# Kernel optimization log

Hardware: AMD Instinct MI355X
Metric: run time of the kernel (lower is better)

The kernel has to match this reference:

```python
import jax, jax.numpy as jnp
import numpy as np

EPS = 1e-5

def setup_inputs() -> dict:
    key = jax.random.key(0)
    ks = jax.random.split(key, 12)
    N, d0, d1, d2, qh, qo = 8192, 128, 256, 256, 128, 1
    state = jax.random.normal(ks[0], (N, d0), dtype=jnp.float32)
    adjacent_matrix = jax.random.uniform(ks[1], (N, N), dtype=jnp.float32)
    s = 0.05
    return {
        "state": state,
        "adjacent_matrix": adjacent_matrix,
        "gamma": jnp.ones((d0,), jnp.float32),
        "beta": jnp.zeros((d0,), jnp.float32),
        "W1": jax.random.normal(ks[2], (d0, d1), jnp.float32) * s,
        "b1": jnp.zeros((d1,), jnp.float32),
        "W2": jax.random.normal(ks[3], (d1, d2), jnp.float32) * s,
        "b2": jnp.zeros((d2,), jnp.float32),
        "Wq1": jax.random.normal(ks[4], (d2, qh), jnp.float32) * s,
        "bq1": jnp.zeros((qh,), jnp.float32),
        "Wq2": jax.random.normal(ks[5], (qh, qo), jnp.float32) * s,
        "bq2": jnp.zeros((qo,), jnp.float32),
    }


def reference(state, adjacent_matrix, gamma, beta, W1, b1, W2, b2, Wq1, bq1, Wq2, bq2):
    # LinkBatchNorm: BatchNorm1d over node (batch) axis, training-mode statistics
    mean = jnp.mean(state, axis=0)
    var = jnp.var(state, axis=0)
    x = (state - mean) * jax.lax.rsqrt(var + EPS) * gamma + beta  # [N, d0]
    # GraphCNN: two layers of relu(A @ X @ W + b)
    h = jax.nn.relu(adjacent_matrix @ (x @ W1) + b1)   # [N, d1]
    h = jax.nn.relu(adjacent_matrix @ (h @ W2) + b2)   # [N, d2]
    # QNetwork: per-node MLP -> Q value
    q = jax.nn.relu(h @ Wq1 + bq1) @ Wq2 + bq2         # [N, 1]
    return q
```

## Files before the change

kernel.cpp:

```cpp
#include <hip/hip_runtime.h>
#include <stdint.h>

#define NN 8192
#define D0 128
#define D1 256
#define D2 256
#define QH 128
#define EPSV 1e-5f

using bf16x8 = __attribute__((ext_vector_type(8))) __bf16;
using f32x4  = __attribute__((ext_vector_type(4))) float;

__device__ __forceinline__ unsigned short f2bf(float f) {
    union { float f; unsigned int u; } v; v.f = f;
    unsigned int r = v.u + 0x7FFFu + ((v.u >> 16) & 1u);
    return (unsigned short)(r >> 16);
}
__device__ __forceinline__ float bf2f(unsigned short h) {
    union { unsigned int u; float f; } v; v.u = ((unsigned int)h) << 16;
    return v.f;
}
__device__ __forceinline__ unsigned pkbf(float a, float b) {
    unsigned r;
    asm("v_cvt_pk_bf16_f32 %0, %1, %2" : "=v"(r) : "v"(a), "v"(b));
    return r;
}
__device__ __forceinline__ void async_ld16(const void* g, void* l) {
    __builtin_amdgcn_global_load_lds(
        (__attribute__((address_space(1))) void*)(g),
        (__attribute__((address_space(3))) void*)(l), 16, 0, 0);
}

__global__ void k_stats(const float* __restrict__ state,
                        float* __restrict__ psum, float* __restrict__ psq,
                        float* __restrict__ acc4k, float* __restrict__ rsA) {
    int j = threadIdx.x;
    int b = blockIdx.x;
    int gid = b * 128 + j;
    if (gid < 8192) rsA[gid] = 0.f;
    if (gid < 1024) acc4k[gid] = 0.f;
    const float* p = state + (size_t)b * 32 * D0 + j;
    float s = 0.f, sq = 0.f;
#pragma unroll 4
    for (int r = 0; r < 32; ++r) { float x = p[(size_t)r * D0]; s += x; sq += x * x; }
    psum[b * D0 + j] = s;
    psq [b * D0 + j] = sq;
}

__global__ void k_finalize(const float* __restrict__ psum, const float* __restrict__ psq,
                           const float* __restrict__ gamma, const float* __restrict__ beta,
                           const float* __restrict__ W1,
                           float* __restrict__ scale, float* __restrict__ shift,
                           float* __restrict__ c1) {
    __shared__ float s_shift[D0];
    int t = threadIdx.x;
    if (t < D0) {
        float s = 0.f, sq = 0.f;
        for (int b = 0; b < 256; ++b) { s += psum[b * D0 + t]; sq += psq[b * D0 + t]; }
        float mean = s * (1.0f / NN);
        float var  = sq * (1.0f / NN) - mean * mean;
        float sc = gamma[t] * rsqrtf(var + EPSV);
        float sh = beta[t] - mean * sc;
        scale[t] = sc; shift[t] = sh; s_shift[t] = sh;
    }
    __syncthreads();
    float acc = 0.f;
    for (int k = 0; k < D0; ++k) acc += s_shift[k] * W1[(size_t)k * D1 + t];
    c1[t] = acc;
}

__global__ void k_prep_weights(const float* __restrict__ W1, const float* __restrict__ W2,
                               const float* __restrict__ scale,
                               unsigned short* __restrict__ W1st,
                               unsigned short* __restrict__ W2t) {
    int idx = blockIdx.x * 256 + threadIdx.x;
    if (idx < 32768) {
        int n = idx >> 7, k = idx & 127;
        W1st[idx] = f2bf(W1[(size_t)k * D1 + n] * scale[k]);
    } else {
        int i = idx - 32768; int n = i >> 8, k = i & 255;
        W2t[i] = f2bf(W2[(size_t)k * D2 + n]);
    }
}

__global__ __launch_bounds__(256) void k_castA_T(const float* __restrict__ A,
                                                 unsigned short* __restrict__ AbfT,
                                                 float* __restrict__ rs) {
    int t = threadIdx.x;
    int row = blockIdx.x * 128 + (t >> 1);
    int off = (t & 1) * 16;
    const float* ap = A + (size_t)row * NN + blockIdx.y * 2048 + off;
    unsigned short* op = AbfT + (size_t)(blockIdx.y * 64) * ((size_t)NN * 32)
                              + (size_t)row * 32 + off;
    const size_t PL = (size_t)NN * 32;
    float s = 0.f;
    for (int kt = 0; kt < 64; ++kt) {
        const float* p = ap + kt * 32;
        float4 v0 = *(const float4*)(p);
        float4 v1 = *(const float4*)(p + 4);
        float4 v2 = *(const float4*)(p + 8);
        float4 v3 = *(const float4*)(p + 12);
        s += v0.x + v0.y + v0.z + v0.w + v1.x + v1.y + v1.z + v1.w
           + v2.x + v2.y + v2.z + v2.w + v3.x + v3.y + v3.z + v3.w;
        uint4 u0 = { pkbf(v0.x, v0.y), pkbf(v0.z, v0.w), pkbf(v1.x, v1.y), pkbf(v1.z, v1.w) };
        uint4 u1 = { pkbf(v2.x, v2.y), pkbf(v2.z, v2.w), pkbf(v3.x, v3.y), pkbf(v3.z, v3.w) };
        *(uint4*)(op + (size_t)kt * PL) = u0;
        *(uint4*)(op + (size_t)kt * PL + 8) = u1;
    }
    s += __shfl_xor(s, 1, 64);
    if ((t & 1) == 0) atomicAdd(rs + row, s);
}

template <int N, int K, bool A_FP32, bool BIAS>
__global__ __launch_bounds__(256, 4) void k_small_gemm(
        const void* __restrict__ Aptr, const unsigned short* __restrict__ Bt,
        const float* __restrict__ bias, unsigned short* __restrict__ out) {
    constexpr int WN = N / 4;
    constexpr int NJ = WN / 16;
    constexpr int BI = N / 64;
    __shared__ unsigned short Alds[32 * 32];
    __shared__ unsigned short Blds[N * 32];
    int t = threadIdx.x, lane = t & 63, w = t >> 6;
    int m0 = blockIdx.x * 32;
    int lr = lane & 15, lk = (lane >> 4) * 8;
    int wc = w * WN;
    f32x4 acc[2][NJ] = {};

    for (int kk = 0; kk < K; kk += 32) {
        __syncthreads();
        if constexpr (A_FP32) {
            const float* A = (const float*)Aptr;
            int row = t >> 3, kc = (t & 7) * 4;
            float4 v = *(const float4*)(A + (size_t)(m0 + row) * K + kk + kc);
            uint2 p;
            p.x = ((unsigned)f2bf(v.y) << 16) | f2bf(v.x);
            p.y = ((unsigned)f2bf(v.w) << 16) | f2bf(v.z);
            *(uint2*)&Alds[row * 32 + kc] = p;
        } else {
            if (w < 2) {
                const unsigned short* A = (const unsigned short*)Aptr;
                int row = w * 16 + (lane >> 2);
                async_ld16(A + (size_t)(m0 + row) * K + kk + (lane & 3) * 8, &Alds[w * 512]);
            }
        }
#pragma unroll
        for (int i = 0; i < BI; ++i) {
            int n = w * WN + i * 16 + (lane >> 2);
            async_ld16(Bt + (size_t)n * K + kk + (lane & 3) * 8, &Blds[(w * WN + i * 16) * 32]);
        }
        __syncthreads();
        bf16x8 a[2], b[NJ];
#pragma unroll
        for (int i = 0; i < 2; ++i) a[i] = *(const bf16x8*)&Alds[(i * 16 + lr) * 32 + lk];
#pragma unroll
        for (int j = 0; j < NJ; ++j) b[j] = *(const bf16x8*)&Blds[(wc + j * 16 + lr) * 32 + lk];
#pragma unroll
        for (int i = 0; i < 2; ++i)
#pragma unroll
            for (int j = 0; j < NJ; ++j)
                acc[i][j] = __builtin_amdgcn_mfma_f32_16x16x32_bf16(a[i], b[j], acc[i][j], 0, 0, 0);
    }
    int q = lane >> 4;
#pragma unroll
    for (int j = 0; j < NJ; ++j) {
        int n = wc + j * 16 + lr;
        float bv = 0.f;
        if constexpr (BIAS) bv = bias[n];
#pragma unroll
        for (int i = 0; i < 2; ++i) {
#pragma unroll
            for (int r = 0; r < 4; ++r) {
                int m = m0 + i * 16 + q * 4 + r;
                out[(size_t)m * N + n] = f2bf(acc[i][j][r] + bv);
            }
        }
    }
}

__global__ void k_transpose(const unsigned short* __restrict__ in, unsigned short* __restrict__ out,
                            float* __restrict__ colsum) {
    __shared__ unsigned short tile[64 * 68];
    __shared__ float cp[4][64];
    int t = threadIdx.x;
    int r0 = blockIdx.x * 64, c0 = blockIdx.y * 64;
#pragma unroll
    for (int p = 0; p < 4; ++p) {
        int row = (t >> 4) + p * 16, col = (t & 15) * 4;
        *(ushort4*)&tile[row * 68 + col] = *(const ushort4*)&in[(size_t)(r0 + row) * 256 + c0 + col];
    }
    __syncthreads();
    int n = t >> 2;
#pragma unroll
    for (int s = 0; s < 2; ++s) {
        int mo = (t & 3) * 16 + s * 8;
        unsigned short v[8];
#pragma unroll
        for (int e = 0; e < 8; ++e) v[e] = tile[(mo + e) * 68 + n];
        int kt = (r0 + mo) >> 5;
        *(uint4*)&out[(size_t)kt * 8192 + (c0 + n) * 32 + (mo & 31)] = *(const uint4*)v;
    }
    int col = t & 63, gg = t >> 6;
    float s = 0.f;
#pragma unroll
    for (int r = 0; r < 16; ++r) s += bf2f(tile[(gg * 16 + r) * 68 + col]);
    cp[gg][col] = s;
    __syncthreads();
    if (t < 64) atomicAdd(colsum + c0 + t, cp[0][t] + cp[1][t] + cp[2][t] + cp[3][t]);
}

__global__ __launch_bounds__(512, 4) void k_big_gemm7(
        const unsigned short* __restrict__ AbfT, const unsigned short* __restrict__ Ytb,
        float* __restrict__ Cp) {
    __shared__ unsigned short Alds[3][128 * 32];
    __shared__ unsigned short Blds[3][256 * 32];
    int t = threadIdx.x, lane = t & 63, w = t >> 6;
    int m0 = blockIdx.x * 128;
    int kt0 = blockIdx.y * 32;
    int wr = (w & 1) * 64, wc = (w >> 1) * 64;
    int lr = lane & 15, q = lane >> 4;
    f32x4 acc[4][4] = {};

    const size_t AS = (size_t)NN * 32;
    const int    BS = 256 * 32;
    int srow = lane >> 2;
    int hsw = (lane & 3) ^ ((srow ^ (srow >> 2)) & 3);
    const unsigned short* agp = AbfT + (size_t)kt0 * AS + (size_t)(m0 + w * 16 + srow) * 32 + hsw * 8;
    const unsigned short* bg0 = Ytb + (size_t)kt0 * BS + (w * 32 + srow) * 32 + hsw * 8;
    const unsigned short* bg1 = bg0 + 16 * 32;
    unsigned short* aL  = &Alds[0][0] + w * 512;
    unsigned short* bL0 = &Blds[0][0] + w * 1024;
    unsigned short* bL1 = bL0 + 512;
    int xsr = (lr ^ (lr >> 2)) & 3;
    int lks = ((q ^ xsr) & 3) * 8;

#pragma unroll
    for (int pt = 0; pt < 2; ++pt) {
        async_ld16(agp + (size_t)pt * AS, aL  + pt * 4096);
        async_ld16(bg0 + (size_t)pt * BS, bL0 + pt * 8192);
        async_ld16(bg1 + (size_t)pt * BS, bL1 + pt * 8192);
    }
    asm volatile("s_waitcnt vmcnt(3)" ::: "memory");
    __builtin_amdgcn_s_barrier();
    __builtin_amdgcn_sched_barrier(0);

    int cur = 0;
#define GEMM7_COMPUTE(BUF)                                                              \
    {                                                                                   \
        const unsigned short* Ab = &Alds[0][0] + (BUF) * 4096;                          \
        const unsigned short* Bb = &Blds[0][0] + (BUF) * 8192;                          \
        bf16x8 a[4];                                                                    \
        _Pragma("unroll")                                                               \
        for (int i = 0; i < 4; ++i) a[i] = *(const bf16x8*)&Ab[(wr + i * 16 + lr) * 32 + lks]; \
        _Pragma("unroll")                                                               \
        for (int j = 0; j < 4; ++j) {                                                   \
            bf16x8 b = *(const bf16x8*)&Bb[(wc + j * 16 + lr) * 32 + lks];              \
            _Pragma("unroll")                                                           \
            for (int i = 0; i < 4; ++i)                                                 \
                acc[i][j] = __builtin_amdgcn_mfma_f32_16x16x32_bf16(a[i], b, acc[i][j], 0, 0, 0); \
        }                                                                               \
    }

#pragma unroll 3
    for (int it = 0; it < 30; ++it) {
        int nb = cur + 2; if (nb >= 3) nb -= 3;
        async_ld16(agp + (size_t)(it + 2) * AS, aL  + nb * 4096);
        async_ld16(bg0 + (size_t)(it + 2) * BS, bL0 + nb * 8192);
        async_ld16(bg1 + (size_t)(it + 2) * BS, bL1 + nb * 8192);
        GEMM7_COMPUTE(cur)
        asm volatile("s_waitcnt vmcnt(3)" ::: "memory");
        __builtin_amdgcn_s_barrier();
        __builtin_amdgcn_sched_barrier(0);
        ++cur; if (cur >= 3) cur = 0;
    }
    GEMM7_COMPUTE(cur)
    asm volatile("s_waitcnt vmcnt(0)" ::: "memory");
    __builtin_amdgcn_s_barrier();
    __builtin_amdgcn_sched_barrier(0);
    ++cur; if (cur >= 3) cur = 0;
    GEMM7_COMPUTE(cur)
#undef GEMM7_COMPUTE

    float* outp = Cp + (size_t)blockIdx.y * NN * 256;
#pragma unroll
    for (int i = 0; i < 4; ++i)
#pragma unroll
        for (int j = 0; j < 4; ++j) {
            int n = wc + j * 16 + lr;
#pragma unroll
            for (int r = 0; r < 4; ++r) {
                int m = m0 + wr + i * 16 + q * 4 + r;
                outp[(size_t)m * 256 + n] = acc[i][j][r];
            }
        }
}

__global__ void k_s2(const float* __restrict__ colB, const float* __restrict__ colH1,
                     const float* __restrict__ W2, float* __restrict__ s2) {
    int n = threadIdx.x;
    float acc = 0.f;
    for (int k = 0; k < 256; ++k) acc += colH1[k] * W2[(size_t)k * 256 + n];
    s2[n] = colB[n] - acc;
}

__global__ __launch_bounds__(256) void k_reduce8(
        const float* __restrict__ Cp, const float* __restrict__ rsA,
        const float* __restrict__ bias, const float* __restrict__ sn,
        unsigned short* __restrict__ out, float* __restrict__ colH1) {
    __shared__ float rs_s[16];
    __shared__ float cs[4][256];
    int t = threadIdx.x;
    int m0 = blockIdx.x * 16;
    const size_t S = (size_t)NN * 256;
    if (t < 16) rs_s[t] = rsA[m0 + t] * (1.0f / 8192.0f);
    __syncthreads();
    int g = t >> 6, cq = (t & 63) * 4;
    float4 snv = *(const float4*)(sn + cq);
    float4 bv  = *(const float4*)(bias + cq);
    float c0 = 0.f, c1a = 0.f, c2 = 0.f, c3 = 0.f;
#pragma unroll
    for (int r4 = 0; r4 < 4; ++r4) {
        int row = g * 4 + r4;
        size_t base = (size_t)(m0 + row) * 256 + cq;
        float4 a = {0.f, 0.f, 0.f, 0.f};
#pragma unroll
        for (int s = 0; s < 8; ++s) {
            float4 p = *(const float4*)(Cp + (size_t)s * S + base);
            a.x += p.x; a.y += p.y; a.z += p.z; a.w += p.w;
        }
        float rsv = rs_s[row];
        float x0 = fmaxf(a.x + bv.x - rsv * snv.x, 0.f);
        float x1 = fmaxf(a.y + bv.y - rsv * snv.y, 0.f);
        float x2 = fmaxf(a.z + bv.z - rsv * snv.z, 0.f);
        float x3 = fmaxf(a.w + bv.w - rsv * snv.w, 0.f);
        ushort4 o; o.x = f2bf(x0); o.y = f2bf(x1); o.z = f2bf(x2); o.w = f2bf(x3);
        *(ushort4*)(out + base) = o;
        c0 += x0; c1a += x1; c2 += x2; c3 += x3;
    }
    cs[g][cq] = c0; cs[g][cq + 1] = c1a; cs[g][cq + 2] = c2; cs[g][cq + 3] = c3;
    __syncthreads();
    float tot = cs[0][t] + cs[1][t] + cs[2][t] + cs[3][t];
    atomicAdd(colH1 + t, tot);
}

__global__ __launch_bounds__(256) void k_reduce_qhead(
        const float* __restrict__ Cp, const float* __restrict__ rsA,
        const float* __restrict__ bias, const float* __restrict__ sn,
        const float* __restrict__ Wq1, const float* __restrict__ bq1,
        const float* __restrict__ Wq2, const float* __restrict__ bq2,
        float* __restrict__ out) {
    __shared__ float sh[16][256];
    __shared__ float rs_s[16];
    __shared__ float red[4][8];
    int t = threadIdx.x;
    int m0 = blockIdx.x * 16;
    const size_t S = (size_t)NN * 256;
    if (t < 16) rs_s[t] = rsA[m0 + t] * (1.0f / 8192.0f);
    __syncthreads();
    int g = t >> 6, cq = (t & 63) * 4;
    float4 snv = *(const float4*)(sn + cq);
    float4 bv  = *(const float4*)(bias + cq);
#pragma unroll
    for (int r4 = 0; r4 < 4; ++r4) {
        int row = g * 4 + r4;
        size_t base = (size_t)(m0 + row) * 256 + cq;
        float4 a = {0.f, 0.f, 0.f, 0.f};
#pragma unroll
        for (int s = 0; s < 8; ++s) {
            float4 p = *(const float4*)(Cp + (size_t)s * S + base);
            a.x += p.x; a.y += p.y; a.z += p.z; a.w += p.w;
        }
        float rsv = rs_s[row];
        float4 o;
        o.x = fmaxf(a.x + bv.x - rsv * snv.x, 0.f);
        o.y = fmaxf(a.y + bv.y - rsv * snv.y, 0.f);
        o.z = fmaxf(a.z + bv.z - rsv * snv.z, 0.f);
        o.w = fmaxf(a.w + bv.w - rsv * snv.w, 0.f);
        *(float4*)&sh[row][cq] = o;
    }
    __syncthreads();
    int h = t & 127, rg = t >> 7;
    float acc[8] = {};
    const float* wq = Wq1 + h;
    for (int n4 = 0; n4 < 64; ++n4) {
        int n = n4 * 4;
        float wa = wq[(size_t)(n + 0) * QH];
        float wb = wq[(size_t)(n + 1) * QH];
        float wcc = wq[(size_t)(n + 2) * QH];
        float wd = wq[(size_t)(n + 3) * QH];
#pragma unroll
        for (int r = 0; r < 8; ++r) {
            float4 sv = *(const float4*)&sh[rg * 8 + r][n];
            acc[r] = fmaf(sv.x, wa, fmaf(sv.y, wb, fmaf(sv.z, wcc, fmaf(sv.w, wd, acc[r]))));
        }
    }
    float b1v = bq1[h], w2v = Wq2[h];
    int wid = t >> 6, lane = t & 63;
#pragma unroll
    for (int r = 0; r < 8; ++r) {
        float v = fmaxf(acc[r] + b1v, 0.f) * w2v;
#pragma unroll
        for (int d = 32; d > 0; d >>= 1) v += __shfl_down(v, d, 64);
        if (lane == 0) red[wid][r] = v;
    }
    __syncthreads();
    if (t < 16) {
        int rg2 = t >> 3, r = t & 7;
        out[m0 + rg2 * 8 + r] = red[rg2 * 2][r] + red[rg2 * 2 + 1][r] + bq2[0];
    }
}

extern "C" void kernel_launch(void* const* d_in, const int* in_sizes, int n_in,
                              void* d_out, int out_size, void* d_ws, size_t ws_size,
                              hipStream_t stream) {
    const float* state = (const float*)d_in[0];
    const float* adj   = (const float*)d_in[1];
    const float* gamma = (const float*)d_in[2];
    const float* beta  = (const float*)d_in[3];
    const float* W1    = (const float*)d_in[4];
    const float* b1    = (const float*)d_in[5];
    const float* W2    = (const float*)d_in[6];
    const float* b2    = (const float*)d_in[7];
    const float* Wq1   = (const float*)d_in[8];
    const float* bq1   = (const float*)d_in[9];
    const float* Wq2   = (const float*)d_in[10];
    const float* bq2   = (const float*)d_in[11];
    float* out = (float*)d_out;

    char* ws = (char*)d_ws;
    float* psum  = (float*)(ws + 0);
    float* psq   = (float*)(ws + 131072);
    float* scale = (float*)(ws + 262144);
    float* shift = (float*)(ws + 262656);
    float* c1    = (float*)(ws + 263168);
    float* colA  = (float*)(ws + 264192);
    float* colB  = (float*)(ws + 265216);
    float* colH1 = (float*)(ws + 266240);
    float* s2    = (float*)(ws + 267264);
    unsigned short* W1st = (unsigned short*)(ws + 268288);
    unsigned short* W2t  = (unsigned short*)(ws + 333824);
    unsigned short* Ybuf = (unsigned short*)(ws + (size_t)1  * (1u << 20));
    unsigned short* Ytb  = (unsigned short*)(ws + (size_t)5  * (1u << 20));
    unsigned short* Hbuf = (unsigned short*)(ws + (size_t)9  * (1u << 20));
    float*          rsA  = (float*)(ws + (size_t)14 * (1u << 20));
    float*          Cp   = (float*)(ws + (size_t)22 * (1u << 20));
    unsigned short* AbfT = (unsigned short*)(ws + (size_t)128 * (1u << 20));

    k_stats<<<256, 128, 0, stream>>>(state, psum, psq, colA, rsA);
    k_finalize<<<1, 256, 0, stream>>>(psum, psq, gamma, beta, W1, scale, shift, c1);
    k_prep_weights<<<384, 256, 0, stream>>>(W1, W2, scale, W1st, W2t);
    k_castA_T<<<dim3(64, 4), 256, 0, stream>>>(adj, AbfT, rsA);

    k_small_gemm<256, 128, true, true><<<256, 256, 0, stream>>>(state, W1st, c1, Ybuf);
    k_transpose<<<dim3(128, 4), 256, 0, stream>>>(Ybuf, Ytb, colA);
    k_big_gemm7<<<dim3(64, 8), 512, 0, stream>>>(AbfT, Ytb, Cp);
    k_reduce8<<<512, 256, 0, stream>>>(Cp, rsA, b1, colA, Hbuf, colH1);

    k_small_gemm<256, 256, false, false><<<256, 256, 0, stream>>>(Hbuf, W2t, nullptr, Ybuf);
    k_transpose<<<dim3(128, 4), 256, 0, stream>>>(Ybuf, Ytb, colB);
    k_s2<<<1, 256, 0, stream>>>(colB, colH1, W2, s2);
    k_big_gemm7<<<dim3(64, 8), 512, 0, stream>>>(AbfT, Ytb, Cp);
    k_reduce_qhead<<<512, 256, 0, stream>>>(Cp, rsA, b2, s2, Wq1, bq1, Wq2, bq2, out);
}
```

Baseline: 613.7 us.

## Replace LDS-staged big GEMM with register-direct global loads and N-split grid

Rewrites the large adjacency GEMM to skip shared-memory staging: each wave loads its bf16 MFMA fragments directly from global memory into registers with a two-stage register double buffer. The block tile shrinks to 128x128 with 256 threads, and a new grid dimension splits the 256 output columns in two. This removes the LDS writes, reads and barriers. In exchange, global/L2 traffic rises because fragments are no longer shared across waves through LDS, and load latency is hidden only by the register prefetch and occupancy.

```diff
diff --git a/kernel.cpp b/kernel.cpp
--- a/kernel.cpp
+++ b/kernel.cpp
@@ -208,84 +208,59 @@
     if (t < 64) atomicAdd(colsum + c0 + t, cp[0][t] + cp[1][t] + cp[2][t] + cp[3][t]);
 }
 
-__global__ __launch_bounds__(512, 4) void k_big_gemm7(
+__global__ __launch_bounds__(256, 3) void k_big_gemm8(
         const unsigned short* __restrict__ AbfT, const unsigned short* __restrict__ Ytb,
         float* __restrict__ Cp) {
-    __shared__ unsigned short Alds[3][128 * 32];
-    __shared__ unsigned short Blds[3][256 * 32];
     int t = threadIdx.x, lane = t & 63, w = t >> 6;
     int m0 = blockIdx.x * 128;
-    int kt0 = blockIdx.y * 32;
+    int n0 = blockIdx.y * 128;
+    int kt0 = blockIdx.z * 32;
     int wr = (w & 1) * 64, wc = (w >> 1) * 64;
     int lr = lane & 15, q = lane >> 4;
     f32x4 acc[4][4] = {};
 
     const size_t AS = (size_t)NN * 32;
-    const int    BS = 256 * 32;
-    int srow = lane >> 2;
-    int hsw = (lane & 3) ^ ((srow ^ (srow >> 2)) & 3);
-    const unsigned short* agp = AbfT + (size_t)kt0 * AS + (size_t)(m0 + w * 16 + srow) * 32 + hsw * 8;
-    const unsigned short* bg0 = Ytb + (size_t)kt0 * BS + (w * 32 + srow) * 32 + hsw * 8;
-    const unsigned short* bg1 = bg0 + 16 * 32;
-    unsigned short* aL  = &Alds[0][0] + w * 512;
-    unsigned short* bL0 = &Blds[0][0] + w * 1024;
-    unsigned short* bL1 = bL0 + 512;
-    int xsr = (lr ^ (lr >> 2)) & 3;
-    int lks = ((q ^ xsr) & 3) * 8;
-
-#pragma unroll
-    for (int pt = 0; pt < 2; ++pt) {
-        async_ld16(agp + (size_t)pt * AS, aL  + pt * 4096);
-        async_ld16(bg0 + (size_t)pt * BS, bL0 + pt * 8192);
-        async_ld16(bg1 + (size_t)pt * BS, bL1 + pt * 8192);
-    }
-    asm volatile("s_waitcnt vmcnt(3)" ::: "memory");
-    __builtin_amdgcn_s_barrier();
-    __builtin_amdgcn_sched_barrier(0);
-
-    int cur = 0;
-#define GEMM7_COMPUTE(BUF)                                                              \
-    {                                                                                   \
-        const unsigned short* Ab = &Alds[0][0] + (BUF) * 4096;                          \
-        const unsigned short* Bb = &Blds[0][0] + (BUF) * 8192;                          \
-        bf16x8 a[4];                                                                    \
-        _Pragma("unroll")                                                               \
-        for (int i = 0; i < 4; ++i) a[i] = *(const bf16x8*)&Ab[(wr + i * 16 + lr) * 32 + lks]; \
-        _Pragma("unroll")                                                               \
-        for (int j = 0; j < 4; ++j) {                                                   \
-            bf16x8 b = *(const bf16x8*)&Bb[(wc + j * 16 + lr) * 32 + lks];              \
-            _Pragma("unroll")                                                           \
-            for (int i = 0; i < 4; ++i)                                                 \
-                acc[i][j] = __builtin_amdgcn_mfma_f32_16x16x32_bf16(a[i], b, acc[i][j], 0, 0, 0); \
-        }                                                                               \
-    }
-
-#pragma unroll 3
-    for (int it = 0; it < 30; ++it) {
-        int nb = cur + 2; if (nb >= 3) nb -= 3;
-        async_ld16(agp + (size_t)(it + 2) * AS, aL  + nb * 4096);
-        async_ld16(bg0 + (size_t)(it + 2) * BS, bL0 + nb * 8192);
-        async_ld16(bg1 + (size_t)(it + 2) * BS, bL1 + nb * 8192);
-        GEMM7_COMPUTE(cur)
-        asm volatile("s_waitcnt vmcnt(3)" ::: "memory");
-        __builtin_amdgcn_s_barrier();
-        __builtin_amdgcn_sched_barrier(0);
-        ++cur; if (cur >= 3) cur = 0;
-    }
-    GEMM7_COMPUTE(cur)
-    asm volatile("s_waitcnt vmcnt(0)" ::: "memory");
-    __builtin_amdgcn_s_barrier();
-    __builtin_amdgcn_sched_barrier(0);
-    ++cur; if (cur >= 3) cur = 0;
-    GEMM7_COMPUTE(cur)
-#undef GEMM7_COMPUTE
-
-    float* outp = Cp + (size_t)blockIdx.y * NN * 256;
+    const size_t BS = 256 * 32;
+    const unsigned short* ag = AbfT + (size_t)kt0 * AS + (size_t)(m0 + wr + lr) * 32 + q * 8;
+    const unsigned short* bg = Ytb  + (size_t)kt0 * BS + (size_t)(n0 + wc + lr) * 32 + q * 8;
+
+#define LD_SET(Av, Bv, KT)                                                               \
+    {                                                                                    \
+        _Pragma("unroll")                                                                \
+        for (int i = 0; i < 4; ++i) Av[i] = *(const bf16x8*)(ag + (size_t)(KT) * AS + i * 512); \
+        _Pragma("unroll")                                                                \
+        for (int j = 0; j < 4; ++j) Bv[j] = *(const bf16x8*)(bg + (size_t)(KT) * BS + j * 512); \
+    }
+
+#define MM_SET(Av, Bv)                                                                   \
+    {                                                                                    \
+        _Pragma("unroll")                                                                \
+        for (int j = 0; j < 4; ++j)                                                      \
+            _Pragma("unroll")                                                            \
+            for (int i = 0; i < 4; ++i)                                                  \
+                acc[i][j] = __builtin_amdgcn_mfma_f32_16x16x32_bf16(Av[i], Bv[j], acc[i][j], 0, 0, 0); \
+    }
+
+    bf16x8 A0[4], B0[4], A1[4], B1[4];
+    LD_SET(A0, B0, 0)
+    for (int it = 0; it < 15; ++it) {
+        LD_SET(A1, B1, 2 * it + 1)
+        MM_SET(A0, B0)
+        LD_SET(A0, B0, 2 * it + 2)
+        MM_SET(A1, B1)
+    }
+    LD_SET(A1, B1, 31)
+    MM_SET(A0, B0)
+    MM_SET(A1, B1)
+#undef LD_SET
+#undef MM_SET
+
+    float* outp = Cp + (size_t)blockIdx.z * NN * 256;
 #pragma unroll
     for (int i = 0; i < 4; ++i)
 #pragma unroll
         for (int j = 0; j < 4; ++j) {
-            int n = wc + j * 16 + lr;
+            int n = n0 + wc + j * 16 + lr;
 #pragma unroll
             for (int r = 0; r < 4; ++r) {
                 int m = m0 + wr + i * 16 + q * 4 + r;
@@ -452,12 +427,12 @@
 
     k_small_gemm<256, 128, true, true><<<256, 256, 0, stream>>>(state, W1st, c1, Ybuf);
     k_transpose<<<dim3(128, 4), 256, 0, stream>>>(Ybuf, Ytb, colA);
-    k_big_gemm7<<<dim3(64, 8), 512, 0, stream>>>(AbfT, Ytb, Cp);
+    k_big_gemm8<<<dim3(64, 2, 8), 256, 0, stream>>>(AbfT, Ytb, Cp);
     k_reduce8<<<512, 256, 0, stream>>>(Cp, rsA, b1, colA, Hbuf, colH1);
 
     k_small_gemm<256, 256, false, false><<<256, 256, 0, stream>>>(Hbuf, W2t, nullptr, Ybuf);
     k_transpose<<<dim3(128, 4), 256, 0, stream>>>(Ybuf, Ytb, colB);
     k_s2<<<1, 256, 0, stream>>>(colB, colH1, W2, s2);
-    k_big_gemm7<<<dim3(64, 8), 512, 0, stream>>>(AbfT, Ytb, Cp);
+    k_big_gemm8<<<dim3(64, 2, 8), 256, 0, stream>>>(AbfT, Ytb, Cp);
     k_reduce_qhead<<<512, 256, 0, stream>>>(Cp, rsA, b2, s2, Wq1, bq1, Wq2, bq2, out);
 }
```

Result: slower. 673.6 us (+9.8%).
